# Kernel optimization log

Measured on AMD Instinct MI355X. Metric: run time of the kernel, lower is better.

Reference implementation:

```python
import jax, jax.numpy as jnp
import numpy as np

C = 128  # n_filters; input channels must equal n_filters due to residual


def setup_inputs() -> dict:
    key = jax.random.key(0)
    kx, kw = jax.random.split(key)
    x = jax.random.normal(kx, (8, 64, 512, C), dtype=jnp.float32)
    # 1x1 conv, no bias == dense over channel axis: [C, 2C]
    W_qkv = jax.random.normal(kw, (C, 2 * C), dtype=jnp.float32) * (1.0 / np.sqrt(C))
    return {"x": x, "W_qkv": W_qkv}


def reference(x, W_qkv):
    # qkv: [B,H,W,2C]; split -> qk [B,H,W,C] -> q,k [B,H,W,C/2]; v [B,H,W,C]
    qkv = jnp.einsum('bhwc,cd->bhwd', x, W_qkv)
    half = C // 2
    q = qkv[..., :half]
    k = qkv[..., half:C]
    v = qkv[..., C:]
    # scores over the W (time) axis; NOTE: original applies no 1/sqrt(d) scaling
    scores = jnp.einsum('bhqc,bhkc->bhqk', q, k)  # [B,H,W,W]
    w = jax.nn.softmax(scores, axis=-1)
    y = jnp.einsum('bhqk,bhkc->bhqc', w, v)  # [B,H,W,C]
    y = x + y  # with_skip_connection=True
    return (y, w)
```

## Files before the change

### kernel.cpp

```cpp
#include <hip/hip_runtime.h>
#include <hip/hip_bf16.h>

typedef short s16x8 __attribute__((ext_vector_type(8)));
typedef float f32x4 __attribute__((ext_vector_type(4)));

#define MFMA_BF16(a,b,c) __builtin_amdgcn_mfma_f32_16x16x32_bf16((a),(b),(c),0,0,0)

static __device__ __forceinline__ unsigned short f2bf(float f){
  unsigned u = __builtin_bit_cast(unsigned, f);
  u += 0x7fffu + ((u >> 16) & 1u);
  return (unsigned short)(u >> 16);
}
static __device__ __forceinline__ float bf2f(unsigned short h){
  unsigned u = ((unsigned)h) << 16;
  return __builtin_bit_cast(float, u);
}
static __device__ __forceinline__ int swzi(int row, int col, int lw){
  const int chunk = (col >> 3) ^ ((row ^ (row >> 3)) & 7);
  return row*lw + (chunk << 3) + (col & 7);
}

__global__ __launch_bounds__(128) void k0_wt(const float* __restrict__ W,
                                             unsigned short* __restrict__ wtH,
                                             unsigned short* __restrict__ wtL){
  const int n = blockIdx.x;
  const int c = threadIdx.x;
  const float v = W[(size_t)c*256 + n];
  const unsigned short h = f2bf(v);
  wtH[n*128 + c] = h;
  wtL[n*128 + c] = f2bf(v - bf2f(h));
}

__global__ __launch_bounds__(512,2) void k1_qkv(const float* __restrict__ x,
    const unsigned short* __restrict__ wtH, const unsigned short* __restrict__ wtL,
    unsigned short* __restrict__ qh, unsigned short* __restrict__ ql,
    unsigned short* __restrict__ kh, unsigned short* __restrict__ kl,
    unsigned short* __restrict__ vT){
  __shared__ unsigned short xh[16384], xl[16384];
  const int t = threadIdx.x;
  const int lane = t & 63, wid = t >> 6;
  const int li = lane & 15, g = lane >> 4;
  const int m0 = blockIdx.x * 128;
  const int wm = wid >> 2, wn = wid & 3;

  {
    const int row = t >> 2, cb = (t & 3) * 32;
    const float* src = x + (size_t)(m0 + row)*128 + cb;
    #pragma unroll
    for (int gg = 0; gg < 4; ++gg){
      const float4 v0 = ((const float4*)src)[2*gg];
      const float4 v1 = ((const float4*)src)[2*gg + 1];
      const float vv[8] = {v0.x,v0.y,v0.z,v0.w,v1.x,v1.y,v1.z,v1.w};
      s16x8 h, l;
      #pragma unroll
      for (int j = 0; j < 8; ++j){
        const unsigned short hb = f2bf(vv[j]);
        h[j] = (short)hb;
        l[j] = (short)f2bf(vv[j] - bf2f(hb));
      }
      const int idx = swzi(row, cb + 8*gg, 128);
      *(s16x8*)&xh[idx] = h;
      *(s16x8*)&xl[idx] = l;
    }
  }
  __syncthreads();

  {
    f32x4 acc[4][2] = {};
    #pragma unroll
    for (int ks = 0; ks < 4; ++ks){
      const int col = ks*32 + g*8;
      s16x8 ah[4], al[4];
      #pragma unroll
      for (int mi = 0; mi < 4; ++mi){
        const int idx = swzi(wm*64 + mi*16 + li, col, 128);
        ah[mi] = *(const s16x8*)&xh[idx];
        al[mi] = *(const s16x8*)&xl[idx];
      }
      #pragma unroll
      for (int ni = 0; ni < 2; ++ni){
        const size_t boff = (size_t)(wn*32 + ni*16 + li)*128 + col;
        const s16x8 bh = *(const s16x8*)(wtH + boff);
        const s16x8 bl = *(const s16x8*)(wtL + boff);
        #pragma unroll
        for (int mi = 0; mi < 4; ++mi){
          acc[mi][ni] = MFMA_BF16(bh, ah[mi], acc[mi][ni]);
          acc[mi][ni] = MFMA_BF16(bh, al[mi], acc[mi][ni]);
          acc[mi][ni] = MFMA_BF16(bl, ah[mi], acc[mi][ni]);
        }
      }
    }
    #pragma unroll
    for (int mi = 0; mi < 4; ++mi)
      #pragma unroll
      for (int ni = 0; ni < 2; ++ni){
        const int pos = m0 + wm*64 + mi*16 + li;
        const int och = wn*32 + ni*16 + g*4;
        ushort4 hv, lv;
        #pragma unroll
        for (int r = 0; r < 4; ++r){
          const float v = acc[mi][ni][r];
          const unsigned short hb = f2bf(v);
          ((unsigned short*)&hv)[r] = hb;
          ((unsigned short*)&lv)[r] = f2bf(v - bf2f(hb));
        }
        const size_t off = (size_t)pos*64 + (och & 63);
        if (wn < 2){ *(ushort4*)&qh[off] = hv; *(ushort4*)&ql[off] = lv; }
        else       { *(ushort4*)&kh[off] = hv; *(ushort4*)&kl[off] = lv; }
      }
  }

  {
    f32x4 acc[4][2] = {};
    #pragma unroll
    for (int ks = 0; ks < 4; ++ks){
      const int col = ks*32 + g*8;
      s16x8 ah[4], al[4];
      #pragma unroll
      for (int mi = 0; mi < 4; ++mi){
        const int idx = swzi(wm*64 + mi*16 + li, col, 128);
        ah[mi] = *(const s16x8*)&xh[idx];
        al[mi] = *(const s16x8*)&xl[idx];
      }
      #pragma unroll
      for (int ni = 0; ni < 2; ++ni){
        const size_t boff = (size_t)(128 + wn*32 + ni*16 + li)*128 + col;
        const s16x8 bh = *(const s16x8*)(wtH + boff);
        const s16x8 bl = *(const s16x8*)(wtL + boff);
        #pragma unroll
        for (int mi = 0; mi < 4; ++mi){
          acc[mi][ni] = MFMA_BF16(ah[mi], bh, acc[mi][ni]);
          acc[mi][ni] = MFMA_BF16(ah[mi], bl, acc[mi][ni]);
          acc[mi][ni] = MFMA_BF16(al[mi], bh, acc[mi][ni]);
        }
      }
    }
    #pragma unroll
    for (int mi = 0; mi < 4; ++mi)
      #pragma unroll
      for (int ni = 0; ni < 2; ++ni){
        const int growb = m0 + wm*64 + mi*16 + g*4;
        const int ch = wn*32 + ni*16 + li;
        const int head = growb >> 9, posb = growb & 511;
        ushort4 pv;
        #pragma unroll
        for (int r = 0; r < 4; ++r)
          ((unsigned short*)&pv)[r] = f2bf(acc[mi][ni][r]);
        *(ushort4*)&vT[((size_t)head << 16) + ch*512 + posb] = pv;
      }
  }
}

__global__ __launch_bounds__(512,2) void k2_attn(
    const unsigned short* __restrict__ qh, const unsigned short* __restrict__ ql,
    const unsigned short* __restrict__ kh, const unsigned short* __restrict__ kl,
    const unsigned short* __restrict__ vT, const float* __restrict__ x,
    float* __restrict__ y, float* __restrict__ wout){
  __shared__ unsigned short wlds[32768];
  __shared__ float redm[512], reds[512];

  const int t = threadIdx.x;
  const int lane = t & 63, wid = t >> 6;
  const int li = lane & 15, g = lane >> 4;
  const int bi = blockIdx.x;
  const int head = (bi & 7) + 8 * (bi >> 6);
  const int qt = (bi >> 3) & 7;
  const size_t hbase = (size_t)head * 512;
  const int q0 = qt * 64;
  const int kbase = wid * 64;

  f32x4 acc[4][4] = {};
  #pragma unroll
  for (int ks = 0; ks < 2; ++ks){
    const int col = ks*32 + g*8;
    s16x8 qbh[4], qbl[4];
    #pragma unroll
    for (int qj = 0; qj < 4; ++qj){
      const size_t aoff = (hbase + q0 + qj*16 + li)*64 + col;
      qbh[qj] = *(const s16x8*)(qh + aoff);
      qbl[qj] = *(const s16x8*)(ql + aoff);
    }
    #pragma unroll
    for (int ni = 0; ni < 4; ++ni){
      const size_t boff = (hbase + kbase + ni*16 + li)*64 + col;
      const s16x8 ah = *(const s16x8*)(kh + boff);
      const s16x8 al = *(const s16x8*)(kl + boff);
      #pragma unroll
      for (int qj = 0; qj < 4; ++qj){
        acc[qj][ni] = MFMA_BF16(ah, qbh[qj], acc[qj][ni]);
        acc[qj][ni] = MFMA_BF16(al, qbh[qj], acc[qj][ni]);
        acc[qj][ni] = MFMA_BF16(ah, qbl[qj], acc[qj][ni]);
      }
    }
  }

  float fsc[4];
  #pragma unroll
  for (int qj = 0; qj < 4; ++qj){
    float m = acc[qj][0][0];
    #pragma unroll
    for (int ni = 0; ni < 4; ++ni)
      #pragma unroll
      for (int r = 0; r < 4; ++r) m = fmaxf(m, acc[qj][ni][r]);
    m = fmaxf(m, __shfl_xor(m, 16));
    m = fmaxf(m, __shfl_xor(m, 32));
    float s = 0.f;
    #pragma unroll
    for (int ni = 0; ni < 4; ++ni)
      #pragma unroll
      for (int r = 0; r < 4; ++r){
        const float e = __expf(acc[qj][ni][r] - m);
        acc[qj][ni][r] = e;
        s += e;
      }
    s += __shfl_xor(s, 16);
    s += __shfl_xor(s, 32);
    if (g == 0){
      redm[(qj*16 + li)*8 + wid] = m;
      reds[(qj*16 + li)*8 + wid] = s;
    }
    fsc[qj] = m;
  }
  __syncthreads();
  #pragma unroll
  for (int qj = 0; qj < 4; ++qj){
    const int row = qj*16 + li;
    const f32x4 m0v = *(const f32x4*)&redm[row*8];
    const f32x4 m1v = *(const f32x4*)&redm[row*8 + 4];
    const f32x4 s0v = *(const f32x4*)&reds[row*8];
    const f32x4 s1v = *(const f32x4*)&reds[row*8 + 4];
    float M = fmaxf(fmaxf(fmaxf(m0v[0], m0v[1]), fmaxf(m0v[2], m0v[3])),
                    fmaxf(fmaxf(m1v[0], m1v[1]), fmaxf(m1v[2], m1v[3])));
    float S = s0v[0]*__expf(m0v[0] - M) + s0v[1]*__expf(m0v[1] - M)
            + s0v[2]*__expf(m0v[2] - M) + s0v[3]*__expf(m0v[3] - M)
            + s1v[0]*__expf(m1v[0] - M) + s1v[1]*__expf(m1v[1] - M)
            + s1v[2]*__expf(m1v[2] - M) + s1v[3]*__expf(m1v[3] - M);
    fsc[qj] = __expf(fsc[qj] - M) / S;
  }

  #pragma unroll
  for (int qj = 0; qj < 4; ++qj){
    const int row = qj*16 + li;
    float* wrow = wout + (hbase + q0 + row)*512;
    #pragma unroll
    for (int ni = 0; ni < 4; ++ni){
      const int col = kbase + ni*16 + g*4;
      f32x4 wv;
      ushort4 pv;
      #pragma unroll
      for (int r = 0; r < 4; ++r){
        const float v = acc[qj][ni][r] * fsc[qj];
        wv[r] = v;
        ((unsigned short*)&pv)[r] = f2bf(v);
      }
      __builtin_nontemporal_store(wv, (f32x4*)&wrow[col]);
      *(ushort4*)&wlds[swzi(row, col, 512)] = pv;
    }
  }
  __syncthreads();

  const int c0 = wid * 16;
  f32x4 yacc[4] = {};
  const unsigned short* vhead = vT + ((size_t)head << 16) + (size_t)(c0 + li)*512;
  #pragma unroll
  for (int kt = 0; kt < 16; ++kt){
    const int kp0 = kt*32 + g*8;
    const s16x8 vb = *(const s16x8*)&vhead[kp0];
    #pragma unroll
    for (int mi = 0; mi < 4; ++mi){
      const s16x8 aw = *(const s16x8*)&wlds[swzi(mi*16 + li, kp0, 512)];
      yacc[mi] = MFMA_BF16(vb, aw, yacc[mi]);
    }
  }

  #pragma unroll
  for (int mi = 0; mi < 4; ++mi){
    const int row = mi*16 + li;
    const size_t idx = (hbase + q0 + row)*128 + c0 + g*4;
    const f32x4 xv = __builtin_nontemporal_load((const f32x4*)&x[idx]);
    f32x4 ov;
    ov[0] = xv[0] + yacc[mi][0];
    ov[1] = xv[1] + yacc[mi][1];
    ov[2] = xv[2] + yacc[mi][2];
    ov[3] = xv[3] + yacc[mi][3];
    __builtin_nontemporal_store(ov, (f32x4*)&y[idx]);
  }
}

extern "C" void kernel_launch(void* const* d_in, const int* in_sizes, int n_in,
                              void* d_out, int out_size, void* d_ws, size_t ws_size,
                              hipStream_t stream){
  (void)in_sizes; (void)n_in; (void)out_size; (void)ws_size;
  const float* x = (const float*)d_in[0];
  const float* W = (const float*)d_in[1];
  float* y    = (float*)d_out;
  float* wout = y + (size_t)33554432;

  char* ws = (char*)d_ws;
  unsigned short* qh  = (unsigned short*)(ws);
  unsigned short* ql  = (unsigned short*)(ws +  33554432ull);
  unsigned short* kh  = (unsigned short*)(ws +  67108864ull);
  unsigned short* kl  = (unsigned short*)(ws + 100663296ull);
  unsigned short* vT  = (unsigned short*)(ws + 134217728ull);
  unsigned short* wtH = (unsigned short*)(ws + 201326592ull);
  unsigned short* wtL = (unsigned short*)(ws + 201392128ull);

  hipLaunchKernelGGL(k0_wt,   dim3(256),  dim3(128), 0, stream, W, wtH, wtL);
  hipLaunchKernelGGL(k1_qkv,  dim3(2048), dim3(512), 0, stream, x, wtH, wtL,
                     qh, ql, kh, kl, vT);
  hipLaunchKernelGGL(k2_attn, dim3(4096), dim3(512), 0, stream,
                     qh, ql, kh, kl, vT, x, y, wout);
}
```

Before: 489.0 us.

## Process whole head per block with V staged once in LDS

The attention kernel now launches one block per head (512 blocks) instead of one per query tile, loads the head's transposed V into LDS once, and loops over the 8 query tiles. The weight tile is staged in two halves to fit LDS alongside V. This avoids re-reading V from global memory for each query tile. In exchange, occupancy drops to one block per CU, there are more barriers per tile, and only 512 blocks are available to fill the GPU.

```diff
diff --git a/kernel.cpp b/kernel.cpp
--- a/kernel.cpp
+++ b/kernel.cpp
@@ -151,139 +151,160 @@
   }
 }
 
-__global__ __launch_bounds__(512,2) void k2_attn(
+__global__ __launch_bounds__(512,1) void k2_attn(
     const unsigned short* __restrict__ qh, const unsigned short* __restrict__ ql,
     const unsigned short* __restrict__ kh, const unsigned short* __restrict__ kl,
     const unsigned short* __restrict__ vT, const float* __restrict__ x,
     float* __restrict__ y, float* __restrict__ wout){
-  __shared__ unsigned short wlds[32768];
-  __shared__ float redm[512], reds[512];
+  __shared__ __align__(16) unsigned short lds[81920];
+  unsigned short* vlds = lds;
+  unsigned short* wlds = lds + 65536;
+  float* redm = (float*)(lds + 65536);
+  float* reds = redm + 512;
 
   const int t = threadIdx.x;
   const int lane = t & 63, wid = t >> 6;
   const int li = lane & 15, g = lane >> 4;
-  const int bi = blockIdx.x;
-  const int head = (bi & 7) + 8 * (bi >> 6);
-  const int qt = (bi >> 3) & 7;
+  const int head = blockIdx.x;
   const size_t hbase = (size_t)head * 512;
-  const int q0 = qt * 64;
   const int kbase = wid * 64;
-
-  f32x4 acc[4][4] = {};
-  #pragma unroll
-  for (int ks = 0; ks < 2; ++ks){
-    const int col = ks*32 + g*8;
-    s16x8 qbh[4], qbl[4];
+  const int c0 = wid * 16;
+
+  {
+    const unsigned short* vsrc = vT + ((size_t)head << 16);
+    #pragma unroll
+    for (int i = 0; i < 16; ++i){
+      const int gi = t + i*512;
+      const int ch = gi >> 6, pb = gi & 63;
+      const s16x8 v = *(const s16x8*)&vsrc[gi*8];
+      *(s16x8*)&vlds[swzi(ch, pb*8, 512)] = v;
+    }
+  }
+  __syncthreads();
+
+  for (int qt = 0; qt < 8; ++qt){
+    const int q0 = qt * 64;
+
+    f32x4 acc[4][4] = {};
+    #pragma unroll
+    for (int ks = 0; ks < 2; ++ks){
+      const int col = ks*32 + g*8;
+      s16x8 qbh[4], qbl[4];
+      #pragma unroll
+      for (int qj = 0; qj < 4; ++qj){
+        const size_t aoff = (hbase + q0 + qj*16 + li)*64 + col;
+        qbh[qj] = *(const s16x8*)(qh + aoff);
+        qbl[qj] = *(const s16x8*)(ql + aoff);
+      }
+      #pragma unroll
+      for (int ni = 0; ni < 4; ++ni){
+        const size_t boff = (hbase + kbase + ni*16 + li)*64 + col;
+        const s16x8 ah = *(const s16x8*)(kh + boff);
+        const s16x8 al = *(const s16x8*)(kl + boff);
+        #pragma unroll
+        for (int qj = 0; qj < 4; ++qj){
+          acc[qj][ni] = MFMA_BF16(ah, qbh[qj], acc[qj][ni]);
+          acc[qj][ni] = MFMA_BF16(al, qbh[qj], acc[qj][ni]);
+          acc[qj][ni] = MFMA_BF16(ah, qbl[qj], acc[qj][ni]);
+        }
+      }
+    }
+
+    float fsc[4];
     #pragma unroll
     for (int qj = 0; qj < 4; ++qj){
-      const size_t aoff = (hbase + q0 + qj*16 + li)*64 + col;
-      qbh[qj] = *(const s16x8*)(qh + aoff);
-      qbl[qj] = *(const s16x8*)(ql + aoff);
-    }
-    #pragma unroll
-    for (int ni = 0; ni < 4; ++ni){
-      const size_t boff = (hbase + kbase + ni*16 + li)*64 + col;
-      const s16x8 ah = *(const s16x8*)(kh + boff);
-      const s16x8 al = *(const s16x8*)(kl + boff);
-      #pragma unroll
-      for (int qj = 0; qj < 4; ++qj){
-        acc[qj][ni] = MFMA_BF16(ah, qbh[qj], acc[qj][ni]);
-        acc[qj][ni] = MFMA_BF16(al, qbh[qj], acc[qj][ni]);
-        acc[qj][ni] = MFMA_BF16(ah, qbl[qj], acc[qj][ni]);
-      }
-    }
-  }
-
-  float fsc[4];
-  #pragma unroll
-  for (int qj = 0; qj < 4; ++qj){
-    float m = acc[qj][0][0];
-    #pragma unroll
-    for (int ni = 0; ni < 4; ++ni)
-      #pragma unroll
-      for (int r = 0; r < 4; ++r) m = fmaxf(m, acc[qj][ni][r]);
-    m = fmaxf(m, __shfl_xor(m, 16));
-    m = fmaxf(m, __shfl_xor(m, 32));
-    float s = 0.f;
-    #pragma unroll
-    for (int ni = 0; ni < 4; ++ni)
-      #pragma unroll
-      for (int r = 0; r < 4; ++r){
-        const float e = __expf(acc[qj][ni][r] - m);
-        acc[qj][ni][r] = e;
-        s += e;
-      }
-    s += __shfl_xor(s, 16);
-    s += __shfl_xor(s, 32);
-    if (g == 0){
-      redm[(qj*16 + li)*8 + wid] = m;
-      reds[(qj*16 + li)*8 + wid] = s;
-    }
-    fsc[qj] = m;
-  }
-  __syncthreads();
-  #pragma unroll
-  for (int qj = 0; qj < 4; ++qj){
-    const int row = qj*16 + li;
-    const f32x4 m0v = *(const f32x4*)&redm[row*8];
-    const f32x4 m1v = *(const f32x4*)&redm[row*8 + 4];
-    const f32x4 s0v = *(const f32x4*)&reds[row*8];
-    const f32x4 s1v = *(const f32x4*)&reds[row*8 + 4];
-    float M = fmaxf(fmaxf(fmaxf(m0v[0], m0v[1]), fmaxf(m0v[2], m0v[3])),
-                    fmaxf(fmaxf(m1v[0], m1v[1]), fmaxf(m1v[2], m1v[3])));
-    float S = s0v[0]*__expf(m0v[0] - M) + s0v[1]*__expf(m0v[1] - M)
-            + s0v[2]*__expf(m0v[2] - M) + s0v[3]*__expf(m0v[3] - M)
-            + s1v[0]*__expf(m1v[0] - M) + s1v[1]*__expf(m1v[1] - M)
-            + s1v[2]*__expf(m1v[2] - M) + s1v[3]*__expf(m1v[3] - M);
-    fsc[qj] = __expf(fsc[qj] - M) / S;
-  }
-
-  #pragma unroll
-  for (int qj = 0; qj < 4; ++qj){
-    const int row = qj*16 + li;
-    float* wrow = wout + (hbase + q0 + row)*512;
-    #pragma unroll
-    for (int ni = 0; ni < 4; ++ni){
-      const int col = kbase + ni*16 + g*4;
-      f32x4 wv;
-      ushort4 pv;
-      #pragma unroll
-      for (int r = 0; r < 4; ++r){
-        const float v = acc[qj][ni][r] * fsc[qj];
-        wv[r] = v;
-        ((unsigned short*)&pv)[r] = f2bf(v);
-      }
-      __builtin_nontemporal_store(wv, (f32x4*)&wrow[col]);
-      *(ushort4*)&wlds[swzi(row, col, 512)] = pv;
-    }
-  }
-  __syncthreads();
-
-  const int c0 = wid * 16;
-  f32x4 yacc[4] = {};
-  const unsigned short* vhead = vT + ((size_t)head << 16) + (size_t)(c0 + li)*512;
-  #pragma unroll
-  for (int kt = 0; kt < 16; ++kt){
-    const int kp0 = kt*32 + g*8;
-    const s16x8 vb = *(const s16x8*)&vhead[kp0];
-    #pragma unroll
-    for (int mi = 0; mi < 4; ++mi){
-      const s16x8 aw = *(const s16x8*)&wlds[swzi(mi*16 + li, kp0, 512)];
-      yacc[mi] = MFMA_BF16(vb, aw, yacc[mi]);
-    }
-  }
-
-  #pragma unroll
-  for (int mi = 0; mi < 4; ++mi){
-    const int row = mi*16 + li;
-    const size_t idx = (hbase + q0 + row)*128 + c0 + g*4;
-    const f32x4 xv = __builtin_nontemporal_load((const f32x4*)&x[idx]);
-    f32x4 ov;
-    ov[0] = xv[0] + yacc[mi][0];
-    ov[1] = xv[1] + yacc[mi][1];
-    ov[2] = xv[2] + yacc[mi][2];
-    ov[3] = xv[3] + yacc[mi][3];
-    __builtin_nontemporal_store(ov, (f32x4*)&y[idx]);
+      float m = acc[qj][0][0];
+      #pragma unroll
+      for (int ni = 0; ni < 4; ++ni)
+        #pragma unroll
+        for (int r = 0; r < 4; ++r) m = fmaxf(m, acc[qj][ni][r]);
+      m = fmaxf(m, __shfl_xor(m, 16));
+      m = fmaxf(m, __shfl_xor(m, 32));
+      float s = 0.f;
+      #pragma unroll
+      for (int ni = 0; ni < 4; ++ni)
+        #pragma unroll
+        for (int r = 0; r < 4; ++r){
+          const float e = __expf(acc[qj][ni][r] - m);
+          acc[qj][ni][r] = e;
+          s += e;
+        }
+      s += __shfl_xor(s, 16);
+      s += __shfl_xor(s, 32);
+      if (g == 0){
+        redm[(qj*16 + li)*8 + wid] = m;
+        reds[(qj*16 + li)*8 + wid] = s;
+      }
+      fsc[qj] = m;
+    }
+    __syncthreads();
+    #pragma unroll
+    for (int qj = 0; qj < 4; ++qj){
+      const int row = qj*16 + li;
+      const f32x4 m0v = *(const f32x4*)&redm[row*8];
+      const f32x4 m1v = *(const f32x4*)&redm[row*8 + 4];
+      const f32x4 s0v = *(const f32x4*)&reds[row*8];
+      const f32x4 s1v = *(const f32x4*)&reds[row*8 + 4];
+      float M = fmaxf(fmaxf(fmaxf(m0v[0], m0v[1]), fmaxf(m0v[2], m0v[3])),
+                      fmaxf(fmaxf(m1v[0], m1v[1]), fmaxf(m1v[2], m1v[3])));
+      float S = s0v[0]*__expf(m0v[0] - M) + s0v[1]*__expf(m0v[1] - M)
+              + s0v[2]*__expf(m0v[2] - M) + s0v[3]*__expf(m0v[3] - M)
+              + s1v[0]*__expf(m1v[0] - M) + s1v[1]*__expf(m1v[1] - M)
+              + s1v[2]*__expf(m1v[2] - M) + s1v[3]*__expf(m1v[3] - M);
+      fsc[qj] = __expf(fsc[qj] - M) / S;
+    }
+    __syncthreads();
+
+    #pragma unroll
+    for (int hf = 0; hf < 2; ++hf){
+      #pragma unroll
+      for (int qj2 = 0; qj2 < 2; ++qj2){
+        const int qj = 2*hf + qj2;
+        const int row = qj*16 + li;
+        const int wrow = qj2*16 + li;
+        float* wr = wout + (hbase + q0 + row)*512;
+        #pragma unroll
+        for (int ni = 0; ni < 4; ++ni){
+          const int col = kbase + ni*16 + g*4;
+          f32x4 wv;
+          ushort4 pv;
+          #pragma unroll
+          for (int r = 0; r < 4; ++r){
+            const float v = acc[qj][ni][r] * fsc[qj];
+            wv[r] = v;
+            ((unsigned short*)&pv)[r] = f2bf(v);
+          }
+          __builtin_nontemporal_store(wv, (f32x4*)&wr[col]);
+          *(ushort4*)&wlds[swzi(wrow, col, 512)] = pv;
+        }
+      }
+      __syncthreads();
+
+      f32x4 yacc[2] = {};
+      #pragma unroll
+      for (int kt = 0; kt < 16; ++kt){
+        const int kp0 = kt*32 + g*8;
+        const s16x8 vb = *(const s16x8*)&vlds[swzi(c0 + li, kp0, 512)];
+        #pragma unroll
+        for (int mi = 0; mi < 2; ++mi){
+          const s16x8 aw = *(const s16x8*)&wlds[swzi(mi*16 + li, kp0, 512)];
+          yacc[mi] = MFMA_BF16(vb, aw, yacc[mi]);
+        }
+      }
+      #pragma unroll
+      for (int mi = 0; mi < 2; ++mi){
+        const int row = hf*32 + mi*16 + li;
+        const size_t idx = (hbase + q0 + row)*128 + c0 + g*4;
+        const f32x4 xv = __builtin_nontemporal_load((const f32x4*)&x[idx]);
+        f32x4 ov;
+        ov[0] = xv[0] + yacc[mi][0];
+        ov[1] = xv[1] + yacc[mi][1];
+        ov[2] = xv[2] + yacc[mi][2];
+        ov[3] = xv[3] + yacc[mi][3];
+        __builtin_nontemporal_store(ov, (f32x4*)&y[idx]);
+      }
+      __syncthreads();
+    }
   }
 }
 
@@ -308,6 +329,6 @@
   hipLaunchKernelGGL(k0_wt,   dim3(256),  dim3(128), 0, stream, W, wtH, wtL);
   hipLaunchKernelGGL(k1_qkv,  dim3(2048), dim3(512), 0, stream, x, wtH, wtL,
                      qh, ql, kh, kl, vT);
-  hipLaunchKernelGGL(k2_attn, dim3(4096), dim3(512), 0, stream,
+  hipLaunchKernelGGL(k2_attn, dim3(512),  dim3(512), 0, stream,
                      qh, ql, kh, kl, vT, x, y, wout);
 }
```

After: 535.8 us. +9.6%, slower.
